# Kernel tuning notes

Hardware: AMD Instinct MI355X
Metric: run time of the kernel (lower is better)

## Reference

```python
import jax, jax.numpy as jnp
import numpy as np
from jax import lax

W_BCE, W_DICE, W_FT, W_HD = 1.0, 1.0, 1.0, 0.1
TV_ALPHA, TV_BETA, TV_GAMMA = 0.7, 0.3, 0.75
HD_MAX_DIST, HD_BK = 10, 3
SMOOTH, EPS, HD_EPS = 1e-6, 1e-7, 1e-8


def _max_pool(x, k):
    # torch F.max_pool2d pads with -inf implicitly
    pad = k // 2
    return lax.reduce_window(x, -jnp.inf, lax.max, (1, 1, k, k), (1, 1, 1, 1),
                             [(0, 0), (0, 0), (pad, pad), (pad, pad)])


def _min_pool(x, k):
    pad = k // 2
    return lax.reduce_window(x, jnp.inf, lax.min, (1, 1, k, k), (1, 1, 1, 1),
                             [(0, 0), (0, 0), (pad, pad), (pad, pad)])


def _soft_boundary(mask, k):
    dil = _max_pool(mask, k)
    ero = _min_pool(mask, k)  # == -max_pool(-mask)
    return jnp.maximum(dil - ero, 0.0)


def _bce_with_logits(logits, target):
    # numerically stable: max(x,0) - x*t + log1p(exp(-|x|))
    return jnp.mean(jnp.maximum(logits, 0.0) - logits * target +
                    jnp.log1p(jnp.exp(-jnp.abs(logits))))


def _dice_loss(probs, target):
    p = probs.reshape(probs.shape[0], -1)
    t = target.reshape(target.shape[0], -1)
    inter = jnp.sum(p * t, axis=1)
    denom = jnp.sum(p, axis=1) + jnp.sum(t, axis=1)
    dice = (2.0 * inter + SMOOTH) / (denom + SMOOTH + EPS)
    return jnp.mean(1.0 - dice)


def _focal_tversky(probs, target):
    p = probs.reshape(probs.shape[0], -1)
    t = target.reshape(target.shape[0], -1)
    TP = jnp.sum(p * t, axis=1)
    FP = jnp.sum(p * (1.0 - t), axis=1)
    FN = jnp.sum((1.0 - p) * t, axis=1)
    tv = (TP + SMOOTH) / (TP + TV_ALPHA * FP + TV_BETA * FN + SMOOTH + EPS)
    return jnp.mean(jnp.power(1.0 - tv, TV_GAMMA))


def _hausdorff_surrogate(probs, target):
    pred_b = _soft_boundary(probs, HD_BK)
    gt_b = _soft_boundary(target, HD_BK)
    total = jnp.zeros((), probs.dtype)
    weight_sum = 0.0
    for d in range(1, HD_MAX_DIST + 1):
        pred_d = _max_pool(pred_b, 2 * d + 1)
        gt_d = _max_pool(gt_b, 2 * d + 1)
        w = float(d) / float(HD_MAX_DIST)
        total = total + w * (jnp.mean(jnp.abs(pred_d - gt_b)) +
                             jnp.mean(jnp.abs(gt_d - pred_b)))
        weight_sum += w
    return total / (weight_sum + HD_EPS)


def setup_inputs() -> dict:
    key = jax.random.key(0)
    k1, k2 = jax.random.split(key)
    B, C, H, W = 16, 1, 512, 512
    logits = jax.random.normal(k1, (B, C, H, W), dtype=jnp.float32)
    target = jax.random.randint(k2, (B, C, H, W), 0, 2, dtype=jnp.int32)
    return {"logits": logits, "target": target}


def reference(logits, target):
    t = target.astype(jnp.float32)
    bce = _bce_with_logits(logits, t)
    probs = jax.nn.sigmoid(logits)
    d = _dice_loss(probs, t)
    ft = _focal_tversky(probs, t)
    hd = _hausdorff_surrogate(probs, t)
    return W_BCE * bce + W_DICE * d + W_FT * ft + W_HD * hd
```

## Files before the change

### kernel.cpp

```cpp
#include <hip/hip_runtime.h>
#include <math.h>

namespace {

constexpr int B = 16, H = 512, W = 512;
constexpr int HWc = H * W;
constexpr size_t Nc = (size_t)B * HWc;

constexpr int NSTRIP = 13;
constexpr int CENT = 42;
constexpr int NBAND = 16;
constexpr int NWORK = NSTRIP * NBAND * B * 2;
constexpr int NSB = NWORK / 4;
constexpr int NBCE = B * 64;

template <int CTRL>
__device__ __forceinline__ float dpp_shift1(float v) {
  int i = __float_as_int(v);
  int r = __builtin_amdgcn_update_dpp(i, i, CTRL, 0xF, 0xF, false);
  return __int_as_float(r);
}

__device__ __forceinline__ float hmax3(float v) {
  return fmaxf(fmaxf(dpp_shift1<0x138>(v), v), dpp_shift1<0x130>(v));
}
__device__ __forceinline__ void hminmax3(float v, float& mx, float& mn) {
  float s1 = dpp_shift1<0x138>(v);
  float s2 = dpp_shift1<0x130>(v);
  mx = fmaxf(fmaxf(s1, v), s2);
  mn = fminf(fminf(s1, v), s2);
}

__device__ __forceinline__ float wave_sum(float v) {
#pragma unroll
  for (int off = 32; off > 0; off >>= 1) v += __shfl_down(v, off);
  return v;
}

__device__ __forceinline__ float block_reduce_256(float v, float* sm, int tid) {
#pragma unroll
  for (int off = 32; off > 0; off >>= 1) v += __shfl_down(v, off);
  int lane = tid & 63, wid = tid >> 6;
  if (lane == 0) sm[wid] = v;
  __syncthreads();
  float r = 0.f;
  if (tid == 0) r = sm[0] + sm[1] + sm[2] + sm[3];
  __syncthreads();
  return r;
}

template <int CH>
__device__ __forceinline__ float load_src(const float* __restrict__ Lg,
                                          const int* __restrict__ Tg, int gy,
                                          int colc) {
  gy = min(max(gy, 0), H - 1);
  if constexpr (CH == 0) {
    float x = Lg[gy * W + colc];
    float e = __expf(-x);
    return __builtin_amdgcn_rcpf(1.f + e);
  } else {
    return (float)Tg[gy * W + colc];
  }
}

template <int D>
__device__ __forceinline__ void dilate_steps(float (&a)[52],
                                             const float (&o)[32],
                                             float (&accv)[4]) {
  if constexpr (D <= 10) {
    float hp = hmax3(a[D - 1]);
    float hc = hmax3(a[D]);
#pragma unroll
    for (int r = D; r <= 51 - D; ++r) {
      float hn = hmax3(a[r + 1]);
      float nv = fmaxf(fmaxf(hp, hc), hn);
      hp = hc;
      hc = hn;
      a[r] = nv;
    }
    constexpr float wd = 0.1f * (float)D;
#pragma unroll
    for (int k = 0; k < 32; ++k) accv[k & 3] += wd * fabsf(a[10 + k] - o[k]);
    dilate_steps<D + 1>(a, o, accv);
  }
}

template <int CH>
__device__ __forceinline__ void fused_body(const float* __restrict__ Lg,
                                           const int* __restrict__ Tg,
                                           int lane, int strip, int band,
                                           int bz,
                                           float* __restrict__ chain_p) {
  int col = strip * CENT - 11 + lane;
  int colc = min(max(col, 0), W - 1);
  int y0 = band * 32;

  float o[32];
  {
    float v0 = load_src<1 - CH>(Lg, Tg, y0 - 1, colc);
    float v1 = load_src<1 - CH>(Lg, Tg, y0, colc);
    float hx0, hn0, hx1, hn1;
    hminmax3(v0, hx0, hn0);
    hminmax3(v1, hx1, hn1);
#pragma unroll
    for (int k = 0; k < 32; ++k) {
      float v2 = load_src<1 - CH>(Lg, Tg, y0 + 1 + k, colc);
      float hx2, hn2;
      hminmax3(v2, hx2, hn2);
      o[k] = fmaxf(fmaxf(hx0, hx1), hx2) - fminf(fminf(hn0, hn1), hn2);
      hx0 = hx1;
      hx1 = hx2;
      hn0 = hn1;
      hn1 = hn2;
    }
  }

  float a[52];
  {
    float v0 = load_src<CH>(Lg, Tg, y0 - 11, colc);
    float v1 = load_src<CH>(Lg, Tg, y0 - 10, colc);
    float hx0, hn0, hx1, hn1;
    hminmax3(v0, hx0, hn0);
    hminmax3(v1, hx1, hn1);
#pragma unroll
    for (int r = 0; r < 52; ++r) {
      float v2 = load_src<CH>(Lg, Tg, y0 - 9 + r, colc);
      float hx2, hn2;
      hminmax3(v2, hx2, hn2);
      a[r] = fmaxf(fmaxf(hx0, hx1), hx2) - fminf(fminf(hn0, hn1), hn2);
      hx0 = hx1;
      hx1 = hx2;
      hn0 = hn1;
      hn1 = hn2;
    }
  }

  float accv[4] = {0.f, 0.f, 0.f, 0.f};
  dilate_steps<1>(a, o, accv);
  float acc = (accv[0] + accv[1]) + (accv[2] + accv[3]);

  bool valid = (lane >= 11 && lane <= 52 && col < W);
  acc = valid ? acc : 0.f;
  acc = wave_sum(acc);
  if (lane == 0) chain_p[(bz * NBAND + band) * NSTRIP + strip] = acc;
}

__device__ __forceinline__ void bce_body(const float* __restrict__ logits,
                                         const int* __restrict__ target,
                                         int blk, float* __restrict__ bceA,
                                         float* __restrict__ spA,
                                         float* __restrict__ stA,
                                         float* __restrict__ sptA) {
  __shared__ float smr[4];
  int img = blk >> 6, seg = blk & 63;
  const float4* L4 =
      (const float4*)(logits + (size_t)img * HWc + (size_t)seg * 4096);
  const int4* T4 =
      (const int4*)(target + (size_t)img * HWc + (size_t)seg * 4096);
  int tid = threadIdx.x;
  float s_bce = 0.f, s_p = 0.f, s_t = 0.f, s_pt = 0.f;
#pragma unroll
  for (int it = 0; it < 4; ++it) {
    float4 x4 = L4[it * 256 + tid];
    int4 t4 = T4[it * 256 + tid];
    float xs[4] = {x4.x, x4.y, x4.z, x4.w};
    int ts[4] = {t4.x, t4.y, t4.z, t4.w};
#pragma unroll
    for (int j = 0; j < 4; ++j) {
      float x = xs[j];
      float tf = (float)ts[j];
      float e = __expf(-x);
      float p = __builtin_amdgcn_rcpf(1.f + e);
      s_p += p;
      s_t += tf;
      s_pt += p * tf;
      s_bce += x * (1.f - tf) + __logf(1.f + e);
    }
  }
  float r;
  r = block_reduce_256(s_bce, smr, tid);
  if (tid == 0) bceA[blk] = r;
  r = block_reduce_256(s_p, smr, tid);
  if (tid == 0) spA[blk] = r;
  r = block_reduce_256(s_t, smr, tid);
  if (tid == 0) stA[blk] = r;
  r = block_reduce_256(s_pt, smr, tid);
  if (tid == 0) sptA[blk] = r;
}

__global__ void __launch_bounds__(256, 4) fused_kernel(
    const float* __restrict__ logits, const int* __restrict__ target,
    float* __restrict__ bceA, float* __restrict__ spA,
    float* __restrict__ stA, float* __restrict__ sptA,
    float* __restrict__ chain_p) {
  if (blockIdx.x < NBCE) {
    bce_body(logits, target, blockIdx.x, bceA, spA, stA, sptA);
    return;
  }
  int tid = threadIdx.x;
  int lane = tid & 63;
  int wv = __builtin_amdgcn_readfirstlane(tid >> 6);
  int widx = (blockIdx.x - NBCE) * 4 + wv;
  int strip = widx % NSTRIP;
  int rest = widx / NSTRIP;
  int band = rest & 15;
  int bz = rest >> 4;
  int img = bz & 15, chain = bz >> 4;
  const float* Lg = logits + (size_t)img * HWc;
  const int* Tg = target + (size_t)img * HWc;
  if (chain == 0)
    fused_body<0>(Lg, Tg, lane, strip, band, bz, chain_p);
  else
    fused_body<1>(Lg, Tg, lane, strip, band, bz, chain_p);
}

__global__ void finalize_kernel(const float* __restrict__ bceA,
                                const float* __restrict__ spA,
                                const float* __restrict__ stA,
                                const float* __restrict__ sptA,
                                const float* __restrict__ chain_p,
                                float* __restrict__ out) {
  __shared__ float smr[4];
  __shared__ float smImg[16][3];
  __shared__ double smd[16][2];
  int tid = threadIdx.x;

  float s = 0.f;
  for (int i = tid; i < NBCE; i += 256) s += bceA[i];
  float bce_sum = block_reduce_256(s, smr, tid);

  s = 0.f;
  for (int i = tid; i < NWORK; i += 256) s += chain_p[i];
  float hd_sum = block_reduce_256(s, smr, tid);

  {
    int img = tid >> 4, part = tid & 15;
    float sp = 0.f, st = 0.f, spt = 0.f;
    for (int j = part; j < 64; j += 16) {
      int idx = img * 64 + j;
      sp += spA[idx];
      st += stA[idx];
      spt += sptA[idx];
    }
#pragma unroll
    for (int off = 8; off > 0; off >>= 1) {
      sp += __shfl_down(sp, off, 16);
      st += __shfl_down(st, off, 16);
      spt += __shfl_down(spt, off, 16);
    }
    if (part == 0) {
      smImg[img][0] = sp;
      smImg[img][1] = st;
      smImg[img][2] = spt;
    }
  }
  __syncthreads();
  if (tid < 16) {
    double sp = smImg[tid][0], st = smImg[tid][1], spt = smImg[tid][2];
    double dice = (2.0 * spt + 1e-6) / (sp + st + 1e-6 + 1e-7);
    double tv = (spt + 1e-6) /
                (spt + 0.7 * (sp - spt) + 0.3 * (st - spt) + 1e-6 + 1e-7);
    smd[tid][0] = 1.0 - dice;
    smd[tid][1] = pow(1.0 - tv, 0.75);
  }
  __syncthreads();
  if (tid == 0) {
    double dice_l = 0.0, ft_l = 0.0;
    for (int i = 0; i < 16; ++i) {
      dice_l += smd[i][0];
      ft_l += smd[i][1];
    }
    dice_l /= 16.0;
    ft_l /= 16.0;
    const double Nd = (double)Nc;
    double bce = (double)bce_sum / Nd;
    double hd = ((double)hd_sum / Nd) / (5.5 + 1e-8);
    out[0] = (float)(bce + dice_l + ft_l + 0.1 * hd);
  }
}

}

extern "C" void kernel_launch(void* const* d_in, const int* in_sizes, int n_in,
                              void* d_out, int out_size, void* d_ws,
                              size_t ws_size, hipStream_t stream) {
  const float* logits = (const float*)d_in[0];
  const int* target = (const int*)d_in[1];
  float* out = (float*)d_out;

  float* part = (float*)d_ws;
  float* bceA = part;
  float* spA = part + NBCE;
  float* stA = part + 2 * NBCE;
  float* sptA = part + 3 * NBCE;
  float* chain_p = part + 4 * NBCE;

  fused_kernel<<<dim3(NBCE + NSB), dim3(256), 0, stream>>>(
      logits, target, bceA, spA, stA, sptA, chain_p);
  finalize_kernel<<<1, 256, 0, stream>>>(bceA, spA, stA, sptA, chain_p, out);
}
```

Before: 136.6 us.

## Split fused kernel into separate BCE and two half-batch stencil kernels

```diff
diff --git a/kernel.cpp b/kernel.cpp
--- a/kernel.cpp
+++ b/kernel.cpp
@@ -11,7 +11,7 @@
 constexpr int CENT = 42;
 constexpr int NBAND = 16;
 constexpr int NWORK = NSTRIP * NBAND * B * 2;
-constexpr int NSB = NWORK / 4;
+constexpr int NSB_HALF = NWORK / 2 / 4;
 constexpr int NBCE = B * 64;
 
 template <int CTRL>
@@ -145,13 +145,45 @@
   if (lane == 0) chain_p[(bz * NBAND + band) * NSTRIP + strip] = acc;
 }
 
-__device__ __forceinline__ void bce_body(const float* __restrict__ logits,
-                                         const int* __restrict__ target,
-                                         int blk, float* __restrict__ bceA,
-                                         float* __restrict__ spA,
-                                         float* __restrict__ stA,
-                                         float* __restrict__ sptA) {
+__device__ __forceinline__ void stencil_dispatch(
+    const float* __restrict__ logits, const int* __restrict__ target,
+    float* __restrict__ chain_p, int img_base, int blk) {
+  int tid = threadIdx.x;
+  int lane = tid & 63;
+  int wv = __builtin_amdgcn_readfirstlane(tid >> 6);
+  int widx = blk * 4 + wv;
+  int strip = widx % NSTRIP;
+  int rest = widx / NSTRIP;
+  int band = rest & 15;
+  int z = rest >> 4;
+  int img = (z & 7) + img_base;
+  int chain = z >> 3;
+  int bz = chain * 16 + img;
+  const float* Lg = logits + (size_t)img * HWc;
+  const int* Tg = target + (size_t)img * HWc;
+  if (chain == 0)
+    fused_body<0>(Lg, Tg, lane, strip, band, bz, chain_p);
+  else
+    fused_body<1>(Lg, Tg, lane, strip, band, bz, chain_p);
+}
+
+__global__ void __launch_bounds__(256, 4) sten_a(
+    const float* __restrict__ logits, const int* __restrict__ target,
+    float* __restrict__ chain_p) {
+  stencil_dispatch(logits, target, chain_p, 0, blockIdx.x);
+}
+__global__ void __launch_bounds__(256, 3) sten_b(
+    const float* __restrict__ logits, const int* __restrict__ target,
+    float* __restrict__ chain_p) {
+  stencil_dispatch(logits, target, chain_p, 8, blockIdx.x);
+}
+
+__global__ void __launch_bounds__(256) bce_kernel(
+    const float* __restrict__ logits, const int* __restrict__ target,
+    float* __restrict__ bceA, float* __restrict__ spA,
+    float* __restrict__ stA, float* __restrict__ sptA) {
   __shared__ float smr[4];
+  int blk = blockIdx.x;
   int img = blk >> 6, seg = blk & 63;
   const float4* L4 =
       (const float4*)(logits + (size_t)img * HWc + (size_t)seg * 4096);
@@ -186,32 +218,6 @@
   if (tid == 0) stA[blk] = r;
   r = block_reduce_256(s_pt, smr, tid);
   if (tid == 0) sptA[blk] = r;
-}
-
-__global__ void __launch_bounds__(256, 4) fused_kernel(
-    const float* __restrict__ logits, const int* __restrict__ target,
-    float* __restrict__ bceA, float* __restrict__ spA,
-    float* __restrict__ stA, float* __restrict__ sptA,
-    float* __restrict__ chain_p) {
-  if (blockIdx.x < NBCE) {
-    bce_body(logits, target, blockIdx.x, bceA, spA, stA, sptA);
-    return;
-  }
-  int tid = threadIdx.x;
-  int lane = tid & 63;
-  int wv = __builtin_amdgcn_readfirstlane(tid >> 6);
-  int widx = (blockIdx.x - NBCE) * 4 + wv;
-  int strip = widx % NSTRIP;
-  int rest = widx / NSTRIP;
-  int band = rest & 15;
-  int bz = rest >> 4;
-  int img = bz & 15, chain = bz >> 4;
-  const float* Lg = logits + (size_t)img * HWc;
-  const int* Tg = target + (size_t)img * HWc;
-  if (chain == 0)
-    fused_body<0>(Lg, Tg, lane, strip, band, bz, chain_p);
-  else
-    fused_body<1>(Lg, Tg, lane, strip, band, bz, chain_p);
 }
 
 __global__ void finalize_kernel(const float* __restrict__ bceA,
@@ -295,7 +301,9 @@
   float* sptA = part + 3 * NBCE;
   float* chain_p = part + 4 * NBCE;
 
-  fused_kernel<<<dim3(NBCE + NSB), dim3(256), 0, stream>>>(
-      logits, target, bceA, spA, stA, sptA, chain_p);
+  bce_kernel<<<dim3(NBCE), dim3(256), 0, stream>>>(logits, target, bceA, spA,
+                                                   stA, sptA);
+  sten_a<<<dim3(NSB_HALF), dim3(256), 0, stream>>>(logits, target, chain_p);
+  sten_b<<<dim3(NSB_HALF), dim3(256), 0, stream>>>(logits, target, chain_p);
   finalize_kernel<<<1, 256, 0, stream>>>(bceA, spA, stA, sptA, chain_p, out);
 }
```

New measurement: 382.3 us. 180% more time.

## Replace finalize kernel with atomic accumulation and last-block combine

Applied to the files above, without the earlier changes.

```diff
diff --git a/kernel.cpp b/kernel.cpp
--- a/kernel.cpp
+++ b/kernel.cpp
@@ -13,6 +13,8 @@
 constexpr int NWORK = NSTRIP * NBAND * B * 2;
 constexpr int NSB = NWORK / 4;
 constexpr int NBCE = B * 64;
+constexpr int NBLOCKS = NSB + NBCE;
+
 
 template <int CTRL>
 __device__ __forceinline__ float dpp_shift1(float v) {
@@ -32,6 +34,12 @@
 }
 
 __device__ __forceinline__ float wave_sum(float v) {
+#pragma unroll
+  for (int off = 32; off > 0; off >>= 1) v += __shfl_down(v, off);
+  return v;
+}
+
+__device__ __forceinline__ double wave_sum_d(double v) {
 #pragma unroll
   for (int off = 32; off > 0; off >>= 1) v += __shfl_down(v, off);
   return v;
@@ -89,8 +97,7 @@
 __device__ __forceinline__ void fused_body(const float* __restrict__ Lg,
                                            const int* __restrict__ Tg,
                                            int lane, int strip, int band,
-                                           int bz,
-                                           float* __restrict__ chain_p) {
+                                           int slot, float* __restrict__ A) {
   int col = strip * CENT - 11 + lane;
   int colc = min(max(col, 0), W - 1);
   int y0 = band * 32;
@@ -142,16 +149,13 @@
   bool valid = (lane >= 11 && lane <= 52 && col < W);
   acc = valid ? acc : 0.f;
   acc = wave_sum(acc);
-  if (lane == 0) chain_p[(bz * NBAND + band) * NSTRIP + strip] = acc;
+  if (lane == 0) atomicAdd(&A[slot], acc);
 }
 
 __device__ __forceinline__ void bce_body(const float* __restrict__ logits,
                                          const int* __restrict__ target,
-                                         int blk, float* __restrict__ bceA,
-                                         float* __restrict__ spA,
-                                         float* __restrict__ stA,
-                                         float* __restrict__ sptA) {
-  __shared__ float smr[4];
+                                         int blk, float* __restrict__ A,
+                                         float* sm) {
   int img = blk >> 6, seg = blk & 63;
   const float4* L4 =
       (const float4*)(logits + (size_t)img * HWc + (size_t)seg * 4096);
@@ -178,105 +182,84 @@
     }
   }
   float r;
-  r = block_reduce_256(s_bce, smr, tid);
-  if (tid == 0) bceA[blk] = r;
-  r = block_reduce_256(s_p, smr, tid);
-  if (tid == 0) spA[blk] = r;
-  r = block_reduce_256(s_t, smr, tid);
-  if (tid == 0) stA[blk] = r;
-  r = block_reduce_256(s_pt, smr, tid);
-  if (tid == 0) sptA[blk] = r;
-}
-
-__global__ void __launch_bounds__(256, 4) fused_kernel(
-    const float* __restrict__ logits, const int* __restrict__ target,
-    float* __restrict__ bceA, float* __restrict__ spA,
-    float* __restrict__ stA, float* __restrict__ sptA,
-    float* __restrict__ chain_p) {
-  if (blockIdx.x < NBCE) {
-    bce_body(logits, target, blockIdx.x, bceA, spA, stA, sptA);
-    return;
-  }
-  int tid = threadIdx.x;
-  int lane = tid & 63;
-  int wv = __builtin_amdgcn_readfirstlane(tid >> 6);
-  int widx = (blockIdx.x - NBCE) * 4 + wv;
-  int strip = widx % NSTRIP;
-  int rest = widx / NSTRIP;
-  int band = rest & 15;
-  int bz = rest >> 4;
-  int img = bz & 15, chain = bz >> 4;
-  const float* Lg = logits + (size_t)img * HWc;
-  const int* Tg = target + (size_t)img * HWc;
-  if (chain == 0)
-    fused_body<0>(Lg, Tg, lane, strip, band, bz, chain_p);
-  else
-    fused_body<1>(Lg, Tg, lane, strip, band, bz, chain_p);
-}
-
-__global__ void finalize_kernel(const float* __restrict__ bceA,
-                                const float* __restrict__ spA,
-                                const float* __restrict__ stA,
-                                const float* __restrict__ sptA,
-                                const float* __restrict__ chain_p,
-                                float* __restrict__ out) {
-  __shared__ float smr[4];
-  __shared__ float smImg[16][3];
-  __shared__ double smd[16][2];
-  int tid = threadIdx.x;
-
-  float s = 0.f;
-  for (int i = tid; i < NBCE; i += 256) s += bceA[i];
-  float bce_sum = block_reduce_256(s, smr, tid);
-
-  s = 0.f;
-  for (int i = tid; i < NWORK; i += 256) s += chain_p[i];
-  float hd_sum = block_reduce_256(s, smr, tid);
-
-  {
-    int img = tid >> 4, part = tid & 15;
-    float sp = 0.f, st = 0.f, spt = 0.f;
-    for (int j = part; j < 64; j += 16) {
-      int idx = img * 64 + j;
-      sp += spA[idx];
-      st += stA[idx];
-      spt += sptA[idx];
-    }
-#pragma unroll
-    for (int off = 8; off > 0; off >>= 1) {
-      sp += __shfl_down(sp, off, 16);
-      st += __shfl_down(st, off, 16);
-      spt += __shfl_down(spt, off, 16);
-    }
-    if (part == 0) {
-      smImg[img][0] = sp;
-      smImg[img][1] = st;
-      smImg[img][2] = spt;
-    }
-  }
-  __syncthreads();
+  r = block_reduce_256(s_bce, sm, tid);
+  if (tid == 0) atomicAdd(&A[64 + (blk & 15)], r);
+  r = block_reduce_256(s_p, sm, tid);
+  if (tid == 0) atomicAdd(&A[80 + img], r);
+  r = block_reduce_256(s_t, sm, tid);
+  if (tid == 0) atomicAdd(&A[96 + img], r);
+  r = block_reduce_256(s_pt, sm, tid);
+  if (tid == 0) atomicAdd(&A[112 + img], r);
+}
+
+__device__ __forceinline__ float coherent_read(float* p) {
+  return atomicAdd(p, 0.f);
+}
+
+__device__ __forceinline__ void combine(float* __restrict__ A,
+                                        float* __restrict__ out, int tid) {
+  if (tid >= 64) return;
+  double v_hd = (double)coherent_read(&A[tid]);
+  v_hd = wave_sum_d(v_hd);
+  double v_bce = (tid < 16) ? (double)coherent_read(&A[64 + tid]) : 0.0;
+  v_bce = wave_sum_d(v_bce);
+  double t_dice = 0.0, t_ft = 0.0;
   if (tid < 16) {
-    double sp = smImg[tid][0], st = smImg[tid][1], spt = smImg[tid][2];
+    double sp = (double)coherent_read(&A[80 + tid]);
+    double st = (double)coherent_read(&A[96 + tid]);
+    double spt = (double)coherent_read(&A[112 + tid]);
     double dice = (2.0 * spt + 1e-6) / (sp + st + 1e-6 + 1e-7);
     double tv = (spt + 1e-6) /
                 (spt + 0.7 * (sp - spt) + 0.3 * (st - spt) + 1e-6 + 1e-7);
-    smd[tid][0] = 1.0 - dice;
-    smd[tid][1] = pow(1.0 - tv, 0.75);
-  }
-  __syncthreads();
+    t_dice = 1.0 - dice;
+    float xs = (float)(1.0 - tv);
+    t_ft = (double)(sqrtf(xs) * sqrtf(sqrtf(xs)));
+  }
+  t_dice = wave_sum_d(t_dice);
+  t_ft = wave_sum_d(t_ft);
   if (tid == 0) {
-    double dice_l = 0.0, ft_l = 0.0;
-    for (int i = 0; i < 16; ++i) {
-      dice_l += smd[i][0];
-      ft_l += smd[i][1];
-    }
-    dice_l /= 16.0;
-    ft_l /= 16.0;
     const double Nd = (double)Nc;
-    double bce = (double)bce_sum / Nd;
-    double hd = ((double)hd_sum / Nd) / (5.5 + 1e-8);
-    out[0] = (float)(bce + dice_l + ft_l + 0.1 * hd);
-  }
+    double bce = v_bce / Nd;
+    double hd = (v_hd / Nd) / (5.5 + 1e-8);
+    out[0] = (float)(bce + t_dice / 16.0 + t_ft / 16.0 + 0.1 * hd);
+  }
+}
+
+__global__ void __launch_bounds__(256, 4) fused_kernel(
+    const float* __restrict__ logits, const int* __restrict__ target,
+    float* __restrict__ A, unsigned* __restrict__ counter,
+    float* __restrict__ out) {
+  __shared__ float sm[4];
+  __shared__ unsigned s_old;
+  int tid = threadIdx.x;
+
+  if (blockIdx.x < NSB) {
+    int lane = tid & 63;
+    int wv = __builtin_amdgcn_readfirstlane(tid >> 6);
+    int widx = blockIdx.x * 4 + wv;
+    int strip = widx % NSTRIP;
+    int rest = widx / NSTRIP;
+    int band = rest & 15;
+    int bz = rest >> 4;
+    int img = bz & 15, chain = bz >> 4;
+    const float* Lg = logits + (size_t)img * HWc;
+    const int* Tg = target + (size_t)img * HWc;
+    int slot = widx & 63;
+    if (chain == 0)
+      fused_body<0>(Lg, Tg, lane, strip, band, slot, A);
+    else
+      fused_body<1>(Lg, Tg, lane, strip, band, slot, A);
+  } else {
+    bce_body(logits, target, blockIdx.x - NSB, A, sm);
+  }
+
+  __syncthreads();
+  if (tid == 0) {
+    __threadfence();
+    s_old = atomicAdd(counter, 1u);
+  }
+  __syncthreads();
+  if (s_old == (unsigned)(NBLOCKS - 1)) combine(A, out, tid);
 }
 
 }
@@ -288,14 +271,11 @@
   const int* target = (const int*)d_in[1];
   float* out = (float*)d_out;
 
-  float* part = (float*)d_ws;
-  float* bceA = part;
-  float* spA = part + NBCE;
-  float* stA = part + 2 * NBCE;
-  float* sptA = part + 3 * NBCE;
-  float* chain_p = part + 4 * NBCE;
-
-  fused_kernel<<<dim3(NBCE + NSB), dim3(256), 0, stream>>>(
-      logits, target, bceA, spA, stA, sptA, chain_p);
-  finalize_kernel<<<1, 256, 0, stream>>>(bceA, spA, stA, sptA, chain_p, out);
-}
+  float* A = (float*)d_ws;
+  unsigned* counter = (unsigned*)(A + 128);
+
+  hipMemsetAsync(d_ws, 0, 1024, stream);
+
+  fused_kernel<<<dim3(NBLOCKS), dim3(256), 0, stream>>>(logits, target, A,
+                                                        counter, out);
+}
```

Measured after the change: 180.4 us. +32.1%, slower.

## Fold finalize kernel into main kernel via last-block atomic counter

Applied to the files above, without the earlier changes.

```diff
diff --git a/kernel.cpp b/kernel.cpp
--- a/kernel.cpp
+++ b/kernel.cpp
@@ -13,6 +13,14 @@
 constexpr int NWORK = NSTRIP * NBAND * B * 2;
 constexpr int NSB = NWORK / 4;
 constexpr int NBCE = B * 64;
+constexpr int NBLOCKS = NSB + NBCE;
+
+__device__ __forceinline__ void astore(float* p, float v) {
+  __hip_atomic_store(p, v, __ATOMIC_RELAXED, __HIP_MEMORY_SCOPE_AGENT);
+}
+__device__ __forceinline__ float aload(const float* p) {
+  return __hip_atomic_load(p, __ATOMIC_RELAXED, __HIP_MEMORY_SCOPE_AGENT);
+}
 
 template <int CTRL>
 __device__ __forceinline__ float dpp_shift1(float v) {
@@ -89,7 +97,7 @@
 __device__ __forceinline__ void fused_body(const float* __restrict__ Lg,
                                            const int* __restrict__ Tg,
                                            int lane, int strip, int band,
-                                           int bz,
+                                           int widx,
                                            float* __restrict__ chain_p) {
   int col = strip * CENT - 11 + lane;
   int colc = min(max(col, 0), W - 1);
@@ -142,7 +150,7 @@
   bool valid = (lane >= 11 && lane <= 52 && col < W);
   acc = valid ? acc : 0.f;
   acc = wave_sum(acc);
-  if (lane == 0) chain_p[(bz * NBAND + band) * NSTRIP + strip] = acc;
+  if (lane == 0) astore(&chain_p[widx], acc);
 }
 
 __device__ __forceinline__ void bce_body(const float* __restrict__ logits,
@@ -150,8 +158,7 @@
                                          int blk, float* __restrict__ bceA,
                                          float* __restrict__ spA,
                                          float* __restrict__ stA,
-                                         float* __restrict__ sptA) {
-  __shared__ float smr[4];
+                                         float* __restrict__ sptA, float* sm) {
   int img = blk >> 6, seg = blk & 63;
   const float4* L4 =
       (const float4*)(logits + (size_t)img * HWc + (size_t)seg * 4096);
@@ -178,59 +185,27 @@
     }
   }
   float r;
-  r = block_reduce_256(s_bce, smr, tid);
-  if (tid == 0) bceA[blk] = r;
-  r = block_reduce_256(s_p, smr, tid);
-  if (tid == 0) spA[blk] = r;
-  r = block_reduce_256(s_t, smr, tid);
-  if (tid == 0) stA[blk] = r;
-  r = block_reduce_256(s_pt, smr, tid);
-  if (tid == 0) sptA[blk] = r;
-}
-
-__global__ void __launch_bounds__(256, 4) fused_kernel(
-    const float* __restrict__ logits, const int* __restrict__ target,
-    float* __restrict__ bceA, float* __restrict__ spA,
-    float* __restrict__ stA, float* __restrict__ sptA,
-    float* __restrict__ chain_p) {
-  if (blockIdx.x < NBCE) {
-    bce_body(logits, target, blockIdx.x, bceA, spA, stA, sptA);
-    return;
-  }
-  int tid = threadIdx.x;
-  int lane = tid & 63;
-  int wv = __builtin_amdgcn_readfirstlane(tid >> 6);
-  int widx = (blockIdx.x - NBCE) * 4 + wv;
-  int strip = widx % NSTRIP;
-  int rest = widx / NSTRIP;
-  int band = rest & 15;
-  int bz = rest >> 4;
-  int img = bz & 15, chain = bz >> 4;
-  const float* Lg = logits + (size_t)img * HWc;
-  const int* Tg = target + (size_t)img * HWc;
-  if (chain == 0)
-    fused_body<0>(Lg, Tg, lane, strip, band, bz, chain_p);
-  else
-    fused_body<1>(Lg, Tg, lane, strip, band, bz, chain_p);
-}
-
-__global__ void finalize_kernel(const float* __restrict__ bceA,
-                                const float* __restrict__ spA,
-                                const float* __restrict__ stA,
-                                const float* __restrict__ sptA,
-                                const float* __restrict__ chain_p,
-                                float* __restrict__ out) {
-  __shared__ float smr[4];
-  __shared__ float smImg[16][3];
-  __shared__ double smd[16][2];
-  int tid = threadIdx.x;
-
+  r = block_reduce_256(s_bce, sm, tid);
+  if (tid == 0) astore(&bceA[blk], r);
+  r = block_reduce_256(s_p, sm, tid);
+  if (tid == 0) astore(&spA[blk], r);
+  r = block_reduce_256(s_t, sm, tid);
+  if (tid == 0) astore(&stA[blk], r);
+  r = block_reduce_256(s_pt, sm, tid);
+  if (tid == 0) astore(&sptA[blk], r);
+}
+
+__device__ __forceinline__ void combine(
+    const float* __restrict__ bceA, const float* __restrict__ spA,
+    const float* __restrict__ stA, const float* __restrict__ sptA,
+    const float* __restrict__ chain_p, float* __restrict__ out, float* smr,
+    float (*smImg)[3], double (*smd)[2], int tid) {
   float s = 0.f;
-  for (int i = tid; i < NBCE; i += 256) s += bceA[i];
+  for (int i = tid; i < NBCE; i += 256) s += aload(&bceA[i]);
   float bce_sum = block_reduce_256(s, smr, tid);
 
   s = 0.f;
-  for (int i = tid; i < NWORK; i += 256) s += chain_p[i];
+  for (int i = tid; i < NWORK; i += 256) s += aload(&chain_p[i]);
   float hd_sum = block_reduce_256(s, smr, tid);
 
   {
@@ -238,9 +213,9 @@
     float sp = 0.f, st = 0.f, spt = 0.f;
     for (int j = part; j < 64; j += 16) {
       int idx = img * 64 + j;
-      sp += spA[idx];
-      st += stA[idx];
-      spt += sptA[idx];
+      sp += aload(&spA[idx]);
+      st += aload(&stA[idx]);
+      spt += aload(&sptA[idx]);
     }
 #pragma unroll
     for (int off = 8; off > 0; off >>= 1) {
@@ -261,7 +236,8 @@
     double tv = (spt + 1e-6) /
                 (spt + 0.7 * (sp - spt) + 0.3 * (st - spt) + 1e-6 + 1e-7);
     smd[tid][0] = 1.0 - dice;
-    smd[tid][1] = pow(1.0 - tv, 0.75);
+    float xs = (float)(1.0 - tv);
+    smd[tid][1] = (double)(sqrtf(xs) * sqrtf(sqrtf(xs)));
   }
   __syncthreads();
   if (tid == 0) {
@@ -279,6 +255,47 @@
   }
 }
 
+__global__ void __launch_bounds__(256, 4) fused_kernel(
+    const float* __restrict__ logits, const int* __restrict__ target,
+    float* __restrict__ bceA, float* __restrict__ spA,
+    float* __restrict__ stA, float* __restrict__ sptA,
+    float* __restrict__ chain_p, unsigned* __restrict__ counter,
+    float* __restrict__ out) {
+  __shared__ float smr[4];
+  __shared__ float smImg[16][3];
+  __shared__ double smd[16][2];
+  __shared__ unsigned s_old;
+  int tid = threadIdx.x;
+
+  if (blockIdx.x < NBCE) {
+    bce_body(logits, target, blockIdx.x, bceA, spA, stA, sptA, smr);
+  } else {
+    int lane = tid & 63;
+    int wv = __builtin_amdgcn_readfirstlane(tid >> 6);
+    int widx = (blockIdx.x - NBCE) * 4 + wv;
+    int strip = widx % NSTRIP;
+    int rest = widx / NSTRIP;
+    int band = rest & 15;
+    int bz = rest >> 4;
+    int img = bz & 15, chain = bz >> 4;
+    const float* Lg = logits + (size_t)img * HWc;
+    const int* Tg = target + (size_t)img * HWc;
+    if (chain == 0)
+      fused_body<0>(Lg, Tg, lane, strip, band, widx, chain_p);
+    else
+      fused_body<1>(Lg, Tg, lane, strip, band, widx, chain_p);
+  }
+
+  __syncthreads();
+  if (tid == 0) {
+    s_old = __hip_atomic_fetch_add(counter, 1u, __ATOMIC_ACQ_REL,
+                                   __HIP_MEMORY_SCOPE_AGENT);
+  }
+  __syncthreads();
+  if (s_old == (unsigned)(NBLOCKS - 1))
+    combine(bceA, spA, stA, sptA, chain_p, out, smr, smImg, smd, tid);
+}
+
 }
 
 extern "C" void kernel_launch(void* const* d_in, const int* in_sizes, int n_in,
@@ -294,8 +311,10 @@
   float* stA = part + 2 * NBCE;
   float* sptA = part + 3 * NBCE;
   float* chain_p = part + 4 * NBCE;
-
-  fused_kernel<<<dim3(NBCE + NSB), dim3(256), 0, stream>>>(
-      logits, target, bceA, spA, stA, sptA, chain_p);
-  finalize_kernel<<<1, 256, 0, stream>>>(bceA, spA, stA, sptA, chain_p, out);
-}
+  unsigned* counter = (unsigned*)(part + 4 * NBCE + NWORK);
+
+  hipMemsetAsync(counter, 0, sizeof(unsigned), stream);
+
+  fused_kernel<<<dim3(NBLOCKS), dim3(256), 0, stream>>>(
+      logits, target, bceA, spA, stA, sptA, chain_p, counter, out);
+}
```

Result: slower. 179.9 us (+31.7%).
